# Optimization experiments

Hardware: AMD Instinct MI355X
Metric: run time of the kernel (lower is better)

Reference implementation:

```python
import jax, jax.numpy as jnp
import numpy as np
from jax import lax

BN_EPS = 1e-5
K_TOP = 2


def _conv_bn_relu_pool(x, w, b, g, beta, mean, var):
    # x: [B,C,H,W], w: [O,I,3,3]; SAME conv -> eval BN -> ReLU -> 2x2 maxpool
    y = lax.conv_general_dilated(x, w, (1, 1), 'SAME',
                                 dimension_numbers=('NCHW', 'OIHW', 'NCHW'))
    y = y + b[None, :, None, None]
    inv = g / jnp.sqrt(var + BN_EPS)
    y = (y - mean[None, :, None, None]) * inv[None, :, None, None] + beta[None, :, None, None]
    y = jax.nn.relu(y)
    return lax.reduce_window(y, -jnp.inf, lax.max, (1, 1, 2, 2), (1, 1, 2, 2), 'VALID')


def setup_inputs() -> dict:
    key = jax.random.key(0)
    ks = jax.random.split(key, 12)
    B, F_DIM, H_DIM, OUT, E = 4096, 128, 64, 10, 8
    d = {}
    d['x'] = jax.random.normal(ks[0], (B, 3, 32, 32), dtype=jnp.float32)
    # conv stacks
    def conv_block(k, cin, cout, i):
        kk = jax.random.split(k, 2)
        d[f'conv{i}_w'] = jax.random.normal(kk[0], (cout, cin, 3, 3), dtype=jnp.float32) * (1.0 / np.sqrt(cin * 9))
        d[f'conv{i}_b'] = jnp.zeros((cout,), dtype=jnp.float32)
        d[f'bn{i}_g'] = jnp.ones((cout,), dtype=jnp.float32)
        d[f'bn{i}_b'] = jnp.zeros((cout,), dtype=jnp.float32)
        d[f'bn{i}_m'] = jax.random.normal(kk[1], (cout,), dtype=jnp.float32) * 0.1
        d[f'bn{i}_v'] = jnp.ones((cout,), dtype=jnp.float32)
    conv_block(ks[1], 3, 32, 1)
    conv_block(ks[2], 32, 64, 2)
    conv_block(ks[3], 64, 128, 3)
    # experts (stacked): MLPHead Linear(128,64) -> ReLU -> Linear(64,10)
    d['w1'] = jax.random.normal(ks[4], (E, F_DIM, H_DIM), dtype=jnp.float32) * (1.0 / np.sqrt(F_DIM))
    d['b1'] = jnp.zeros((E, H_DIM), dtype=jnp.float32)
    d['w2'] = jax.random.normal(ks[5], (E, H_DIM, OUT), dtype=jnp.float32) * (1.0 / np.sqrt(H_DIM))
    d['b2'] = jnp.zeros((E, OUT), dtype=jnp.float32)
    # top-k gate: Linear(128, 8)
    d['gate_w'] = jax.random.normal(ks[6], (F_DIM, E), dtype=jnp.float32) * (1.0 / np.sqrt(F_DIM))
    d['gate_b'] = jnp.zeros((E,), dtype=jnp.float32)
    return d


def reference(x, conv1_w, conv1_b, bn1_g, bn1_b, bn1_m, bn1_v,
              conv2_w, conv2_b, bn2_g, bn2_b, bn2_m, bn2_v,
              conv3_w, conv3_b, bn3_g, bn3_b, bn3_m, bn3_v,
              w1, b1, w2, b2, gate_w, gate_b):
    # Backbone: 3x32x32 -> 128 (eval-mode BN, dropout identity)
    h = _conv_bn_relu_pool(x, conv1_w, conv1_b, bn1_g, bn1_b, bn1_m, bn1_v)  # [B,32,16,16]
    h = _conv_bn_relu_pool(h, conv2_w, conv2_b, bn2_g, bn2_b, bn2_m, bn2_v)  # [B,64,8,8]
    h = _conv_bn_relu_pool(h, conv3_w, conv3_b, bn3_g, bn3_b, bn3_m, bn3_v)  # [B,128,4,4]
    feat = jnp.mean(h, axis=(2, 3))  # AdaptiveAvgPool2d(1) + Flatten -> [B,128]

    # Top-k gate: logits -> top-k -> softmax over selected -> scatter to [B,E]
    logits = feat @ gate_w + gate_b                     # [B,E]
    vals, idx = lax.top_k(logits, K_TOP)                # [B,k]
    wk = jax.nn.softmax(vals, axis=-1)                  # [B,k]
    B, E = logits.shape
    weights = jnp.zeros((B, E), dtype=logits.dtype)
    weights = weights.at[jnp.arange(B)[:, None], idx].set(wk)

    # Dense expert MLPs (as in source), gate-weighted sum
    he = jax.nn.relu(jnp.einsum('bf,efh->beh', feat, w1) + b1[None])  # [B,E,H]
    oe = jnp.einsum('beh,eho->beo', he, w2) + b2[None]                # [B,E,O]
    return jnp.einsum('be,beo->bo', weights, oe)                      # [B,O]
```

## Files before the change

### kernel.cpp

```cpp
#include <hip/hip_runtime.h>
#include <math.h>

typedef __attribute__((ext_vector_type(8))) short short8;
typedef __attribute__((ext_vector_type(4))) float f32x4;
#define MFMA __builtin_amdgcn_mfma_f32_16x16x32_bf16

#define BN_EPS 1e-5f

static const size_t W1C2_OFF = 0;
static const size_t W2C2_OFF = 1024;
static const size_t W3C2_OFF = 19456;
static const size_t B1_OFF   = 93184;
static const size_t B2_OFF   = 93216;
static const size_t B3_OFF   = 93280;

__device__ inline unsigned short rneb(float x) {
    unsigned u = __float_as_uint(x);
    return (unsigned short)((u + 0x7FFFu + ((u >> 16) & 1u)) >> 16);
}
__device__ inline float b2f(unsigned short h) {
    return __uint_as_float(((unsigned)h) << 16);
}

__global__ __launch_bounds__(256) void k_prep(
    const float* __restrict__ c1w, const float* __restrict__ c2w, const float* __restrict__ c3w,
    const float* __restrict__ c1b, const float* __restrict__ g1, const float* __restrict__ be1,
    const float* __restrict__ m1, const float* __restrict__ v1,
    const float* __restrict__ c2b, const float* __restrict__ g2, const float* __restrict__ be2,
    const float* __restrict__ m2, const float* __restrict__ v2,
    const float* __restrict__ c3b, const float* __restrict__ g3, const float* __restrict__ be3,
    const float* __restrict__ m3, const float* __restrict__ v3,
    unsigned short* __restrict__ w1c2, unsigned short* __restrict__ w2c2,
    unsigned short* __restrict__ w3c2,
    float* __restrict__ b1c, float* __restrict__ b2c, float* __restrict__ b3c)
{
    int i = blockIdx.x * 256 + threadIdx.x;
    if (i < 2048) {
        int e = i & 7, p = (i >> 3) & 1, kc = (i >> 4) & 3, ol = (i >> 6) & 15, n = i >> 10;
        int o = n * 16 + ol, k = kc * 8 + e;
        float s = g1[o] * rsqrtf(v1[o] + BN_EPS);
        float wv = (k < 27) ? c1w[o * 27 + k] * s : 0.f;
        unsigned short h = rneb(wv);
        w1c2[i] = p ? rneb(wv - b2f(h)) : h;
        return;
    }
    i -= 2048;
    if (i < 36864) {
        int e = i & 7, p = (i >> 3) & 1, kc = (i >> 4) & 3, ol = (i >> 6) & 15;
        int n = (i >> 10) & 3, tap = i >> 12;
        int o = n * 16 + ol, ci = kc * 8 + e;
        float s = g2[o] * rsqrtf(v2[o] + BN_EPS);
        float wv = c2w[o * 288 + ci * 9 + tap] * s;
        unsigned short h = rneb(wv);
        w2c2[i] = p ? rneb(wv - b2f(h)) : h;
        return;
    }
    i -= 36864;
    if (i < 147456) {
        int e = i & 7, p = (i >> 3) & 1, kc = (i >> 4) & 3, ol = (i >> 6) & 15;
        int nf = (i >> 10) & 7, s_ = (i >> 13) & 1, tap = i >> 14;
        int o = nf * 16 + ol, ci = s_ * 32 + kc * 8 + e;
        float sc = g3[o] * rsqrtf(v3[o] + BN_EPS);
        float wv = c3w[o * 576 + ci * 9 + tap] * sc;
        unsigned short h = rneb(wv);
        w3c2[i] = p ? rneb(wv - b2f(h)) : h;
        return;
    }
    i -= 147456;
    if (i < 32) { float s = g1[i]*rsqrtf(v1[i]+BN_EPS); b1c[i] = (c1b[i]-m1[i])*s + be1[i]; return; }
    i -= 32;
    if (i < 64) { float s = g2[i]*rsqrtf(v2[i]+BN_EPS); b2c[i] = (c2b[i]-m2[i])*s + be2[i]; return; }
    i -= 64;
    if (i < 128) { float s = g3[i]*rsqrtf(v3[i]+BN_EPS); b3c[i] = (c3b[i]-m3[i])*s + be3[i]; return; }
}

__global__ __launch_bounds__(512, 4) void k_fused(
    const float* __restrict__ x,
    const unsigned short* __restrict__ w1c2,
    const unsigned short* __restrict__ w2c2,
    const unsigned short* __restrict__ w3c2,
    const float* __restrict__ b1c, const float* __restrict__ b2c, const float* __restrict__ b3c,
    const float* __restrict__ w1e, const float* __restrict__ b1e,
    const float* __restrict__ w2e, const float* __restrict__ b2e,
    const float* __restrict__ gw, const float* __restrict__ gb,
    float* __restrict__ out)
{
    __shared__ __align__(16) unsigned short R1[20736];
    __shared__ __align__(16) unsigned int   R2x[3074];
    float* sFeat = (float*)R2x;
    float* sOutB = (float*)R2x + 128;
    float* sPart = (float*)R2x + 160;

    const int b = blockIdx.x, t = threadIdx.x;
    const int lane = t & 63, w = t >> 6;
    const int l15 = lane & 15, lg = lane >> 4;
    const int4 z4 = {0, 0, 0, 0};

    {
        const float* xb = x + (size_t)b * 3072;
        for (int i = t; i < 3072; i += 512) {
            float v = xb[i];
            unsigned short h = rneb(v);
            unsigned short lo = rneb(v - b2f(h));
            R2x[i] = ((unsigned)h << 16) | lo;
        }
        if (t == 0) R2x[3072] = 0;
        for (int hh = t; hh < 272; hh += 512) {
            int pr = hh >> 2, kc = hh & 3;
            int py, px;
            if (pr < 36) { py = (pr < 18) ? 0 : 17; px = (pr < 18) ? pr : pr - 18; }
            else { int r = pr - 36; py = 1 + (r >> 1); px = (r & 1) ? 17 : 0; }
            int ei = ((py * 4 + kc) * 18 + px) * 8;
            *(int4*)(R1 + ei) = z4;
            *(int4*)(R1 + 10368 + ei) = z4;
        }
    }
    __syncthreads();

    {
        short8 b1h[2], b1l[2];
#pragma unroll
        for (int n = 0; n < 2; n++) {
            const short8* bp = (const short8*)(w1c2 + 16 * ((n * 16 + l15) * 4 + lg));
            b1h[n] = bp[0]; b1l[n] = bp[1];
        }
        int dyE[8], dxE[8], cbE[8];
#pragma unroll
        for (int e = 0; e < 8; e++) {
            int k = lg * 8 + e;
            if (k < 27) { int ci = k / 9, tp = k - ci * 9;
                          dyE[e] = tp / 3 - 1; dxE[e] = tp % 3 - 1; cbE[e] = ci << 10; }
            else { dyE[e] = -1000; dxE[e] = 0; cbE[e] = 0; }
        }
        float bia[2] = { b1c[l15], b1c[16 + l15] };
#pragma unroll 1
        for (int q = 0; q < 2; q++) {
            int m0 = 8 * w + 4 * q;
            f32x4 acc[4][2];
#pragma unroll
            for (int mi = 0; mi < 4; mi++)
#pragma unroll
                for (int n = 0; n < 2; n++) acc[mi][n] = (f32x4)0.f;
#pragma unroll
            for (int mi = 0; mi < 4; mi++) {
                int pos = 16 * (m0 + mi) + l15, py = pos >> 5, px = pos & 31;
                short8 ah, al;
#pragma unroll
                for (int e = 0; e < 8; e++) {
                    int yy = py + dyE[e], xv = px + dxE[e];
                    int idx = cbE[e] + (yy << 5) + xv;
                    bool ok = ((unsigned)yy < 32u) && ((unsigned)xv < 32u);
                    unsigned u = R2x[ok ? idx : 3072];
                    ah[e] = (short)(u >> 16);
                    al[e] = (short)(u & 0xFFFFu);
                }
#pragma unroll
                for (int n = 0; n < 2; n++) {
                    acc[mi][n] = MFMA(ah, b1h[n], acc[mi][n], 0, 0, 0);
                    acc[mi][n] = MFMA(ah, b1l[n], acc[mi][n], 0, 0, 0);
                    acc[mi][n] = MFMA(al, b1h[n], acc[mi][n], 0, 0, 0);
                }
            }
            int PY = 2 * w + q;
#pragma unroll
            for (int n = 0; n < 2; n++) {
                int o = n * 16 + l15;
#pragma unroll
                for (int h = 0; h < 2; h++)
#pragma unroll
                for (int jp = 0; jp < 2; jp++) {
                    float v00 = fmaxf(acc[h][n][2*jp]     + bia[n], 0.f);
                    float v01 = fmaxf(acc[h][n][2*jp + 1] + bia[n], 0.f);
                    float v10 = fmaxf(acc[h+2][n][2*jp]     + bia[n], 0.f);
                    float v11 = fmaxf(acc[h+2][n][2*jp + 1] + bia[n], 0.f);
                    float pm = fmaxf(fmaxf(v00, v01), fmaxf(v10, v11));
                    int PX = h * 8 + lg * 2 + jp;
                    unsigned short ph = rneb(pm), pl = rneb(pm - b2f(ph));
                    int ei = (((PY + 1) * 4 + (o >> 3)) * 18 + (PX + 1)) * 8 + (o & 7);
                    R1[ei] = ph; R1[10368 + ei] = pl;
                }
            }
        }
    }
    __syncthreads();

    {
        const int mh = w & 1, nn = w >> 1;
        f32x4 acc2[8];
#pragma unroll
        for (int mi = 0; mi < 8; mi++) acc2[mi] = (f32x4)0.f;
        const unsigned short* wb = w2c2 + ((size_t)(nn * 16 + l15) * 4 + lg) * 16;
        const int abase = (mh * 8) * 576 + lg * 144 + l15 * 8;
        short8 bhA, blA, bhB, blB;
#define LDB2(tp, BH, BL) { const short8* bp = (const short8*)(wb + (tp) * 4096); BH = bp[0]; BL = bp[1]; }
#define CMP2(tp, BH, BL) { int dy_ = (tp) / 3, dx_ = (tp) - 3 * dy_; \
        int roff_ = dy_ * 576 + dx_ * 8; \
        _Pragma("unroll") for (int mi = 0; mi < 8; mi++) { \
            int ea_ = abase + mi * 576 + roff_; \
            short8 ah_ = *(const short8*)(R1 + ea_); \
            short8 al_ = *(const short8*)(R1 + 10368 + ea_); \
            acc2[mi] = MFMA(ah_, BH, acc2[mi], 0, 0, 0); \
            acc2[mi] = MFMA(ah_, BL, acc2[mi], 0, 0, 0); \
            acc2[mi] = MFMA(al_, BH, acc2[mi], 0, 0, 0); } }
        LDB2(0, bhA, blA);
#pragma unroll 1
        for (int tp = 0; tp < 8; tp += 2) {
            LDB2(tp + 1, bhB, blB);
            CMP2(tp, bhA, blA);
            LDB2(tp + 2, bhA, blA);
            CMP2(tp + 1, bhB, blB);
        }
        CMP2(8, bhA, blA);
        __syncthreads();
        for (int hh = t; hh < 288; hh += 512) {
            int pr = hh >> 3, kc = hh & 7;
            int py, px;
            if (pr < 20) { py = (pr < 10) ? 0 : 9; px = (pr < 10) ? pr : pr - 10; }
            else { int r = pr - 20; py = 1 + (r >> 1); px = (r & 1) ? 9 : 0; }
            int ei = ((py * 8 + kc) * 11 + px) * 8;
            *(int4*)(R1 + ei) = z4;
            *(int4*)(R1 + 7040 + ei) = z4;
        }
        {
            int o = nn * 16 + l15;
            float bia = b2c[o];
#pragma unroll
            for (int mi2 = 0; mi2 < 4; mi2++) {
                int PY = mh * 4 + mi2;
#pragma unroll
                for (int jp = 0; jp < 2; jp++) {
                    float v00 = fmaxf(acc2[2*mi2][2*jp]     + bia, 0.f);
                    float v01 = fmaxf(acc2[2*mi2][2*jp + 1] + bia, 0.f);
                    float v10 = fmaxf(acc2[2*mi2+1][2*jp]     + bia, 0.f);
                    float v11 = fmaxf(acc2[2*mi2+1][2*jp + 1] + bia, 0.f);
                    float pm = fmaxf(fmaxf(v00, v01), fmaxf(v10, v11));
                    int PX = lg * 2 + jp;
                    unsigned short ph = rneb(pm), pl = rneb(pm - b2f(ph));
                    int ei = (((PY + 1) * 8 + (o >> 3)) * 11 + (PX + 1)) * 8 + (o & 7);
                    R1[ei] = ph; R1[7040 + ei] = pl;
                }
            }
        }
    }
    __syncthreads();

    {
        const int nf = w;
        f32x4 acc3[4];
#pragma unroll
        for (int mi = 0; mi < 4; mi++) acc3[mi] = (f32x4)0.f;
        const unsigned short* wb3 = w3c2 + ((size_t)(nf * 16 + l15) * 4 + lg) * 16;
        const int py0 = (l15 >> 3), px3 = l15 & 7;
        short8 bhA, blA, bhB, blB;
#define LDB3(ii, BH, BL) { const short8* bp = (const short8*)(wb3 + (ii) * 8192); BH = bp[0]; BL = bp[1]; }
#define CMP3(ii, BH, BL) { int tap_ = (ii) >> 1, s_ = (ii) & 1; \
        int dy_ = tap_ / 3, dx_ = tap_ - 3 * dy_; \
        int roff_ = dy_ * 704 + (s_ * 4 + lg) * 88 + dx_ * 8 + px3 * 8; \
        _Pragma("unroll") for (int mi = 0; mi < 4; mi++) { \
            int ea_ = (mi * 2 + py0) * 704 + roff_; \
            short8 ah_ = *(const short8*)(R1 + ea_); \
            short8 al_ = *(const short8*)(R1 + 7040 + ea_); \
            acc3[mi] = MFMA(ah_, BH, acc3[mi], 0, 0, 0); \
            acc3[mi] = MFMA(ah_, BL, acc3[mi], 0, 0, 0); \
            acc3[mi] = MFMA(al_, BH, acc3[mi], 0, 0, 0); } }
        LDB3(0, bhA, blA);
#pragma unroll 1
        for (int ii = 0; ii < 16; ii += 2) {
            LDB3(ii + 1, bhB, blB);
            CMP3(ii, bhA, blA);
            LDB3(ii + 2, bhA, blA);
            CMP3(ii + 1, bhB, blB);
        }
        LDB3(17, bhB, blB);
        CMP3(16, bhA, blA);
        CMP3(17, bhB, blB);
        {
            int o = nf * 16 + l15;
            float bia = b3c[o];
            float featsum = 0.f;
#pragma unroll
            for (int mi = 0; mi < 4; mi++) {
                float sumv = 0.f;
#pragma unroll
                for (int jp = 0; jp < 2; jp++) {
                    float v0 = fmaxf(acc3[mi][2*jp]     + bia, 0.f);
                    float v1 = fmaxf(acc3[mi][2*jp + 1] + bia, 0.f);
                    float vm = fmaxf(v0, v1);
                    vm = fmaxf(vm, __shfl_xor(vm, 32, 64));
                    sumv += vm;
                }
                sumv += __shfl_xor(sumv, 16, 64);
                featsum += sumv;
            }
            if (lane < 16) sFeat[nf * 16 + lane] = featsum * (1.0f / 16.0f);
        }
    }
    __syncthreads();

    int i1 = 0, i2 = 0;
    float wk1 = 0.f, wk2 = 0.f;
    {
        float f0 = sFeat[lane], f1 = sFeat[64 + lane];
        float lgt[8];
#pragma unroll
        for (int e = 0; e < 8; e++) {
            float p = f0 * gw[lane * 8 + e] + f1 * gw[(64 + lane) * 8 + e];
#pragma unroll
            for (int s = 1; s < 64; s <<= 1) p += __shfl_xor(p, s, 64);
            lgt[e] = p + gb[e];
        }
        float v1m = -1e30f, v2m = -1e30f;
#pragma unroll
        for (int e = 0; e < 8; e++) {
            float le = lgt[e];
            if (le > v1m) { v2m = v1m; i2 = i1; v1m = le; i1 = e; }
            else if (le > v2m) { v2m = le; i2 = e; }
        }
        float ex = expf(v2m - v1m);
        wk1 = 1.f / (1.f + ex); wk2 = ex / (1.f + ex);
        int e = (w < 4) ? i1 : i2;
        int k0 = (w & 3) * 32;
        const float* W1 = w1e + (size_t)e * 8192 + (size_t)k0 * 64;
        float hj = 0.f;
#pragma unroll 8
        for (int kk = 0; kk < 32; kk++) hj += sFeat[k0 + kk] * W1[kk * 64 + lane];
        sPart[w * 64 + lane] = hj;
    }
    __syncthreads();
    if (w < 2) {
        int e = (w == 0) ? i1 : i2;
        float wk = (w == 0) ? wk1 : wk2;
        float hj = b1e[e * 64 + lane]
                 + sPart[(w * 4 + 0) * 64 + lane] + sPart[(w * 4 + 1) * 64 + lane]
                 + sPart[(w * 4 + 2) * 64 + lane] + sPart[(w * 4 + 3) * 64 + lane];
        hj = fmaxf(hj, 0.f);
        const float* W2 = w2e + (size_t)e * 640 + lane * 10;
#pragma unroll
        for (int o = 0; o < 10; o++) {
            float po = hj * W2[o];
#pragma unroll
            for (int s = 1; s < 64; s <<= 1) po += __shfl_xor(po, s, 64);
            if (lane == 0) sOutB[w * 10 + o] = wk * (po + b2e[e * 10 + o]);
        }
    }
    __syncthreads();
    if (t < 10) out[(size_t)b * 10 + t] = sOutB[t] + sOutB[10 + t];
}

extern "C" void kernel_launch(void* const* d_in, const int* in_sizes, int n_in,
                              void* d_out, int out_size, void* d_ws, size_t ws_size,
                              hipStream_t stream)
{
    const float* x   = (const float*)d_in[0];
    const float* c1w = (const float*)d_in[1];
    const float* c1b = (const float*)d_in[2];
    const float* g1  = (const float*)d_in[3];
    const float* be1 = (const float*)d_in[4];
    const float* m1  = (const float*)d_in[5];
    const float* v1  = (const float*)d_in[6];
    const float* c2w = (const float*)d_in[7];
    const float* c2b = (const float*)d_in[8];
    const float* g2  = (const float*)d_in[9];
    const float* be2 = (const float*)d_in[10];
    const float* m2  = (const float*)d_in[11];
    const float* v2  = (const float*)d_in[12];
    const float* c3w = (const float*)d_in[13];
    const float* c3b = (const float*)d_in[14];
    const float* g3  = (const float*)d_in[15];
    const float* be3 = (const float*)d_in[16];
    const float* m3  = (const float*)d_in[17];
    const float* v3  = (const float*)d_in[18];
    const float* w1e = (const float*)d_in[19];
    const float* b1e = (const float*)d_in[20];
    const float* w2e = (const float*)d_in[21];
    const float* b2e = (const float*)d_in[22];
    const float* gw  = (const float*)d_in[23];
    const float* gb  = (const float*)d_in[24];

    float* ws = (float*)d_ws;
    unsigned short* w1c2 = (unsigned short*)(ws + W1C2_OFF);
    unsigned short* w2c2 = (unsigned short*)(ws + W2C2_OFF);
    unsigned short* w3c2 = (unsigned short*)(ws + W3C2_OFF);
    float* b1c = ws + B1_OFF;
    float* b2c = ws + B2_OFF;
    float* b3c = ws + B3_OFF;

    k_prep<<<729, 256, 0, stream>>>(c1w, c2w, c3w,
                                    c1b, g1, be1, m1, v1,
                                    c2b, g2, be2, m2, v2,
                                    c3b, g3, be3, m3, v3,
                                    w1c2, w2c2, w3c2, b1c, b2c, b3c);
    k_fused<<<4096, 512, 0, stream>>>(x, w1c2, w2c2, w3c2, b1c, b2c, b3c,
                                      w1e, b1e, w2e, b2e, gw, gb, (float*)d_out);
}
```

Before: 295.2 us.

## Re-tile conv2/conv3 MFMA work so waves reuse activations across output channels

Conv2 now gives each wave two output rows across all 64 output channels instead of eight M-tiles for one 16-channel slice. Conv3 now gives each wave one spatial M-tile with four N-tiles instead of all spatial tiles for one channel group. Each activation fragment loaded from LDS is therefore reused across several weight fragments, which cuts LDS traffic, while weight fragments are read from global/L2 more often and the manual double-buffered prefetch is dropped. Conv3 also now needs an extra partial-feature reduction pass and barrier, with feature buffers moved to new shared offsets.

```diff
diff --git a/kernel.cpp b/kernel.cpp
--- a/kernel.cpp
+++ b/kernel.cpp
@@ -3,7 +3,7 @@
 
 typedef __attribute__((ext_vector_type(8))) short short8;
 typedef __attribute__((ext_vector_type(4))) float f32x4;
-#define MFMA __builtin_amdgcn_mfma_f32_16x16x32_bf16
+#define MFMA16 __builtin_amdgcn_mfma_f32_16x16x32_bf16
 
 #define BN_EPS 1e-5f
 
@@ -87,9 +87,9 @@
 {
     __shared__ __align__(16) unsigned short R1[20736];
     __shared__ __align__(16) unsigned int   R2x[3074];
-    float* sFeat = (float*)R2x;
-    float* sOutB = (float*)R2x + 128;
-    float* sPart = (float*)R2x + 160;
+    float* sFeatP = (float*)R2x;
+    float* sPart  = (float*)R2x + 512;
+    float* sOutB  = (float*)R2x + 1024;
 
     const int b = blockIdx.x, t = threadIdx.x;
     const int lane = t & 63, w = t >> 6;
@@ -156,9 +156,9 @@
                 }
 #pragma unroll
                 for (int n = 0; n < 2; n++) {
-                    acc[mi][n] = MFMA(ah, b1h[n], acc[mi][n], 0, 0, 0);
-                    acc[mi][n] = MFMA(ah, b1l[n], acc[mi][n], 0, 0, 0);
-                    acc[mi][n] = MFMA(al, b1h[n], acc[mi][n], 0, 0, 0);
+                    acc[mi][n] = MFMA16(ah, b1h[n], acc[mi][n], 0, 0, 0);
+                    acc[mi][n] = MFMA16(ah, b1l[n], acc[mi][n], 0, 0, 0);
+                    acc[mi][n] = MFMA16(al, b1h[n], acc[mi][n], 0, 0, 0);
                 }
             }
             int PY = 2 * w + q;
@@ -185,59 +185,65 @@
     __syncthreads();
 
     {
-        const int mh = w & 1, nn = w >> 1;
-        f32x4 acc2[8];
-#pragma unroll
-        for (int mi = 0; mi < 8; mi++) acc2[mi] = (f32x4)0.f;
-        const unsigned short* wb = w2c2 + ((size_t)(nn * 16 + l15) * 4 + lg) * 16;
-        const int abase = (mh * 8) * 576 + lg * 144 + l15 * 8;
-        short8 bhA, blA, bhB, blB;
-#define LDB2(tp, BH, BL) { const short8* bp = (const short8*)(wb + (tp) * 4096); BH = bp[0]; BL = bp[1]; }
-#define CMP2(tp, BH, BL) { int dy_ = (tp) / 3, dx_ = (tp) - 3 * dy_; \
-        int roff_ = dy_ * 576 + dx_ * 8; \
-        _Pragma("unroll") for (int mi = 0; mi < 8; mi++) { \
-            int ea_ = abase + mi * 576 + roff_; \
-            short8 ah_ = *(const short8*)(R1 + ea_); \
-            short8 al_ = *(const short8*)(R1 + 10368 + ea_); \
-            acc2[mi] = MFMA(ah_, BH, acc2[mi], 0, 0, 0); \
-            acc2[mi] = MFMA(ah_, BL, acc2[mi], 0, 0, 0); \
-            acc2[mi] = MFMA(al_, BH, acc2[mi], 0, 0, 0); } }
-        LDB2(0, bhA, blA);
-#pragma unroll 1
-        for (int tp = 0; tp < 8; tp += 2) {
-            LDB2(tp + 1, bhB, blB);
-            CMP2(tp, bhA, blA);
-            LDB2(tp + 2, bhA, blA);
-            CMP2(tp + 1, bhB, blB);
-        }
-        CMP2(8, bhA, blA);
+        const int rw = 2 * w;
+        f32x4 acc2[2][4];
+#pragma unroll
+        for (int mi = 0; mi < 2; mi++)
+#pragma unroll
+            for (int n = 0; n < 4; n++) acc2[mi][n] = (f32x4)0.f;
+        const int abase = rw * 576 + lg * 144 + l15 * 8;
+#pragma unroll
+        for (int tap = 0; tap < 9; tap++) {
+            const int dy = tap / 3, dx = tap - 3 * (tap / 3);
+            const int roff = dy * 576 + dx * 8;
+            short8 ah0, al0, ah1, al1;
+            {
+                int ea = abase + roff;
+                ah0 = *(const short8*)(R1 + ea);
+                al0 = *(const short8*)(R1 + 10368 + ea);
+                ea += 576;
+                ah1 = *(const short8*)(R1 + ea);
+                al1 = *(const short8*)(R1 + 10368 + ea);
+            }
+#pragma unroll
+            for (int n = 0; n < 4; n++) {
+                const short8* bp = (const short8*)(w2c2 + (size_t)tap * 4096
+                                                   + ((n * 16 + l15) * 4 + lg) * 16);
+                short8 bh = bp[0], bl = bp[1];
+                acc2[0][n] = MFMA16(ah0, bh, acc2[0][n], 0, 0, 0);
+                acc2[0][n] = MFMA16(ah0, bl, acc2[0][n], 0, 0, 0);
+                acc2[0][n] = MFMA16(al0, bh, acc2[0][n], 0, 0, 0);
+                acc2[1][n] = MFMA16(ah1, bh, acc2[1][n], 0, 0, 0);
+                acc2[1][n] = MFMA16(ah1, bl, acc2[1][n], 0, 0, 0);
+                acc2[1][n] = MFMA16(al1, bh, acc2[1][n], 0, 0, 0);
+            }
+        }
         __syncthreads();
         for (int hh = t; hh < 288; hh += 512) {
             int pr = hh >> 3, kc = hh & 7;
             int py, px;
             if (pr < 20) { py = (pr < 10) ? 0 : 9; px = (pr < 10) ? pr : pr - 10; }
-            else { int r = pr - 20; py = 1 + (r >> 1); px = (r & 1) ? 9 : 0; }
+            else { int rr = pr - 20; py = 1 + (rr >> 1); px = (rr & 1) ? 9 : 0; }
             int ei = ((py * 8 + kc) * 11 + px) * 8;
             *(int4*)(R1 + ei) = z4;
             *(int4*)(R1 + 7040 + ei) = z4;
         }
         {
-            int o = nn * 16 + l15;
-            float bia = b2c[o];
-#pragma unroll
-            for (int mi2 = 0; mi2 < 4; mi2++) {
-                int PY = mh * 4 + mi2;
+#pragma unroll
+            for (int n = 0; n < 4; n++) {
+                int oc = n * 16 + l15;
+                float bia = b2c[oc];
 #pragma unroll
                 for (int jp = 0; jp < 2; jp++) {
-                    float v00 = fmaxf(acc2[2*mi2][2*jp]     + bia, 0.f);
-                    float v01 = fmaxf(acc2[2*mi2][2*jp + 1] + bia, 0.f);
-                    float v10 = fmaxf(acc2[2*mi2+1][2*jp]     + bia, 0.f);
-                    float v11 = fmaxf(acc2[2*mi2+1][2*jp + 1] + bia, 0.f);
+                    float v00 = fmaxf(acc2[0][n][2*jp]     + bia, 0.f);
+                    float v01 = fmaxf(acc2[0][n][2*jp + 1] + bia, 0.f);
+                    float v10 = fmaxf(acc2[1][n][2*jp]     + bia, 0.f);
+                    float v11 = fmaxf(acc2[1][n][2*jp + 1] + bia, 0.f);
                     float pm = fmaxf(fmaxf(v00, v01), fmaxf(v10, v11));
                     int PX = lg * 2 + jp;
-                    unsigned short ph = rneb(pm), pl = rneb(pm - b2f(ph));
-                    int ei = (((PY + 1) * 8 + (o >> 3)) * 11 + (PX + 1)) * 8 + (o & 7);
-                    R1[ei] = ph; R1[7040 + ei] = pl;
+                    unsigned short ph = rneb(pm);
+                    int ei = (((w + 1) * 8 + (oc >> 3)) * 11 + (PX + 1)) * 8 + (oc & 7);
+                    R1[ei] = ph; R1[7040 + ei] = rneb(pm - b2f(ph));
                 }
             }
         }
@@ -245,62 +251,56 @@
     __syncthreads();
 
     {
-        const int nf = w;
+        const int mt = w >> 1, nh = w & 1;
         f32x4 acc3[4];
 #pragma unroll
-        for (int mi = 0; mi < 4; mi++) acc3[mi] = (f32x4)0.f;
-        const unsigned short* wb3 = w3c2 + ((size_t)(nf * 16 + l15) * 4 + lg) * 16;
-        const int py0 = (l15 >> 3), px3 = l15 & 7;
-        short8 bhA, blA, bhB, blB;
-#define LDB3(ii, BH, BL) { const short8* bp = (const short8*)(wb3 + (ii) * 8192); BH = bp[0]; BL = bp[1]; }
-#define CMP3(ii, BH, BL) { int tap_ = (ii) >> 1, s_ = (ii) & 1; \
-        int dy_ = tap_ / 3, dx_ = tap_ - 3 * dy_; \
-        int roff_ = dy_ * 704 + (s_ * 4 + lg) * 88 + dx_ * 8 + px3 * 8; \
-        _Pragma("unroll") for (int mi = 0; mi < 4; mi++) { \
-            int ea_ = (mi * 2 + py0) * 704 + roff_; \
-            short8 ah_ = *(const short8*)(R1 + ea_); \
-            short8 al_ = *(const short8*)(R1 + 7040 + ea_); \
-            acc3[mi] = MFMA(ah_, BH, acc3[mi], 0, 0, 0); \
-            acc3[mi] = MFMA(ah_, BL, acc3[mi], 0, 0, 0); \
-            acc3[mi] = MFMA(al_, BH, acc3[mi], 0, 0, 0); } }
-        LDB3(0, bhA, blA);
-#pragma unroll 1
-        for (int ii = 0; ii < 16; ii += 2) {
-            LDB3(ii + 1, bhB, blB);
-            CMP3(ii, bhA, blA);
-            LDB3(ii + 2, bhA, blA);
-            CMP3(ii + 1, bhB, blB);
-        }
-        LDB3(17, bhB, blB);
-        CMP3(16, bhA, blA);
-        CMP3(17, bhB, blB);
-        {
-            int o = nf * 16 + l15;
-            float bia = b3c[o];
-            float featsum = 0.f;
-#pragma unroll
-            for (int mi = 0; mi < 4; mi++) {
-                float sumv = 0.f;
-#pragma unroll
-                for (int jp = 0; jp < 2; jp++) {
-                    float v0 = fmaxf(acc3[mi][2*jp]     + bia, 0.f);
-                    float v1 = fmaxf(acc3[mi][2*jp + 1] + bia, 0.f);
-                    float vm = fmaxf(v0, v1);
-                    vm = fmaxf(vm, __shfl_xor(vm, 32, 64));
-                    sumv += vm;
-                }
-                sumv += __shfl_xor(sumv, 16, 64);
-                featsum += sumv;
-            }
-            if (lane < 16) sFeat[nf * 16 + lane] = featsum * (1.0f / 16.0f);
-        }
-    }
+        for (int q = 0; q < 4; q++) acc3[q] = (f32x4)0.f;
+        const int py0 = l15 >> 3, px3 = l15 & 7;
+        const int arow = mt * 2 + py0;
+#pragma unroll
+        for (int ii = 0; ii < 18; ii++) {
+            const int tap = ii >> 1, s = ii & 1;
+            const int dy = tap / 3, dx = tap - 3 * (tap / 3);
+            int ea = (arow + dy) * 704 + (s * 4 + lg) * 88 + (px3 + dx) * 8;
+            short8 ah = *(const short8*)(R1 + ea);
+            short8 al = *(const short8*)(R1 + 7040 + ea);
+#pragma unroll
+            for (int q = 0; q < 4; q++) {
+                const int nf = nh * 4 + q;
+                const short8* bp = (const short8*)(w3c2 + (size_t)ii * 8192
+                                                   + ((nf * 16 + l15) * 4 + lg) * 16);
+                short8 bh = bp[0], bl = bp[1];
+                acc3[q] = MFMA16(ah, bh, acc3[q], 0, 0, 0);
+                acc3[q] = MFMA16(ah, bl, acc3[q], 0, 0, 0);
+                acc3[q] = MFMA16(al, bh, acc3[q], 0, 0, 0);
+            }
+        }
+#pragma unroll
+        for (int q = 0; q < 4; q++) {
+            int oc = (nh * 4 + q) * 16 + l15;
+            float bia = b3c[oc];
+            float fs = 0.f;
+#pragma unroll
+            for (int jp = 0; jp < 2; jp++) {
+                float v0 = fmaxf(acc3[q][2*jp]     + bia, 0.f);
+                float v1 = fmaxf(acc3[q][2*jp + 1] + bia, 0.f);
+                float vm = fmaxf(v0, v1);
+                vm = fmaxf(vm, __shfl_xor(vm, 32, 64));
+                fs += vm;
+            }
+            fs += __shfl_xor(fs, 16, 64);
+            if (lane < 16) sFeatP[mt * 128 + oc] = fs;
+        }
+    }
+    __syncthreads();
+    if (t < 128) sFeatP[t] = (sFeatP[t] + sFeatP[128 + t] + sFeatP[256 + t]
+                              + sFeatP[384 + t]) * (1.0f / 16.0f);
     __syncthreads();
 
     int i1 = 0, i2 = 0;
     float wk1 = 0.f, wk2 = 0.f;
     {
-        float f0 = sFeat[lane], f1 = sFeat[64 + lane];
+        float f0 = sFeatP[lane], f1 = sFeatP[64 + lane];
         float lgt[8];
 #pragma unroll
         for (int e = 0; e < 8; e++) {
@@ -323,7 +323,7 @@
         const float* W1 = w1e + (size_t)e * 8192 + (size_t)k0 * 64;
         float hj = 0.f;
 #pragma unroll 8
-        for (int kk = 0; kk < 32; kk++) hj += sFeat[k0 + kk] * W1[kk * 64 + lane];
+        for (int kk = 0; kk < 32; kk++) hj += sFeatP[k0 + kk] * W1[kk * 64 + lane];
         sPart[w * 64 + lane] = hj;
     }
     __syncthreads();
```

After: 846.6 us. +186.8%, slower.
